# Optimization experiments

Measured on AMD Instinct MI355X. Metric: run time of the kernel, lower is better.

Reference implementation:

```python
import jax, jax.numpy as jnp
import numpy as np

N, T, F, H = 20000, 64, 32, 64
E = 640000
G1, G2 = 64, 32


def _lstm_layer(x_seq, Wih, Whh, bih, bhh):
    # x_seq: [N, T, Fin] -> hs [N, T, H], PyTorch gate order i,f,g,o
    n, _, _ = x_seq.shape
    h_dim = Whh.shape[1]
    h0 = jnp.zeros((n, h_dim), x_seq.dtype)
    c0 = jnp.zeros((n, h_dim), x_seq.dtype)

    def step(carry, xt):
        h, c = carry
        gates = xt @ Wih.T + h @ Whh.T + bih + bhh
        i, f, g, o = jnp.split(gates, 4, axis=-1)
        c = jax.nn.sigmoid(f) * c + jax.nn.sigmoid(i) * jnp.tanh(g)
        h = jax.nn.sigmoid(o) * jnp.tanh(c)
        return (h, c), h

    (_, _), hs = jax.lax.scan(step, (h0, c0), jnp.swapaxes(x_seq, 0, 1))
    return jnp.swapaxes(hs, 0, 1)


def _gcn(h, src, dst, W, b):
    # GCNConv (PyG default): add self-loops, symmetric deg^-1/2 normalization
    n = h.shape[0]
    loop = jnp.arange(n)
    s = jnp.concatenate([src, loop])
    d = jnp.concatenate([dst, loop])
    deg = jax.ops.segment_sum(jnp.ones_like(d, dtype=h.dtype), d, num_segments=n)
    dinv = jnp.where(deg > 0, deg ** -0.5, 0.0)
    norm = dinv[s] * dinv[d]
    xw = h @ W                      # [n, out]
    msg = xw[s] * norm[:, None]     # gather on source nodes
    return jax.ops.segment_sum(msg, d, num_segments=n) + b


def setup_inputs() -> dict:
    key = jax.random.key(0)
    ks = jax.random.split(key, 16)
    s = 0.1
    inp = {
        "x": jax.random.normal(ks[0], (N, T, F), jnp.float32),
        "stock_ids": jax.random.randint(ks[1], (N,), 0, N),
        "edge_index": jax.random.randint(ks[2], (2, E), 0, N),
        # LSTM layer 0
        "Wih0": jax.random.normal(ks[3], (4 * H, F), jnp.float32) * s,
        "Whh0": jax.random.normal(ks[4], (4 * H, H), jnp.float32) * s,
        "bih0": jnp.zeros((4 * H,), jnp.float32),
        "bhh0": jnp.zeros((4 * H,), jnp.float32),
        # LSTM layer 1
        "Wih1": jax.random.normal(ks[5], (4 * H, H), jnp.float32) * s,
        "Whh1": jax.random.normal(ks[6], (4 * H, H), jnp.float32) * s,
        "bih1": jnp.zeros((4 * H,), jnp.float32),
        "bhh1": jnp.zeros((4 * H,), jnp.float32),
        # GCN layers
        "gcn1_W": jax.random.normal(ks[7], (H, G1), jnp.float32) * s,
        "gcn1_b": jnp.zeros((G1,), jnp.float32),
        "gcn2_W": jax.random.normal(ks[8], (G1, G2), jnp.float32) * s,
        "gcn2_b": jnp.zeros((G2,), jnp.float32),
        # head
        "fc_W": jax.random.normal(ks[9], (1, G2), jnp.float32) * s,
        "fc_b": jnp.zeros((1,), jnp.float32),
    }
    return inp


def reference(x, stock_ids, edge_index, Wih0, Whh0, bih0, bhh0,
              Wih1, Whh1, bih1, bhh1, gcn1_W, gcn1_b, gcn2_W, gcn2_b,
              fc_W, fc_b):
    # 2-layer LSTM (eval mode: inter-layer dropout is identity)
    h1 = _lstm_layer(x, Wih0, Whh0, bih0, bhh0)
    h2 = _lstm_layer(h1, Wih1, Whh1, bih1, bhh1)
    h = h2[:, -1, :]                              # [N, H]
    src, dst = edge_index[0], edge_index[1]
    g = jax.nn.relu(_gcn(h, src, dst, gcn1_W, gcn1_b))
    g = jax.nn.relu(_gcn(g, src, dst, gcn2_W, gcn2_b))
    node_features = g[stock_ids]                  # [B, 32]
    out = node_features @ fc_W.T + fc_b           # [B, 1]
    return out.squeeze(-1)
```

## Files before the change

### kernel.cpp

```cpp
#include <hip/hip_runtime.h>
#include <math.h>

#define TT 64
#define FF 32
#define HH 64
#define NN 16
#define GG1 64
#define GG2 32

typedef float f32x4 __attribute__((ext_vector_type(4)));
typedef short bf16x8 __attribute__((ext_vector_type(8)));

__device__ __forceinline__ float fexp2(float x){ return __builtin_amdgcn_exp2f(x); }
__device__ __forceinline__ float frcp (float x){ return __builtin_amdgcn_rcpf(x); }
#define L2E 1.442695041f
__device__ __forceinline__ float sigm_nb(float v, float nb){
  return frcp(1.0f + fexp2(fmaf(v, -L2E, nb)));
}
__device__ __forceinline__ float tanh_b(float v, float b2){
  return fmaf(-2.0f, frcp(1.0f + fexp2(fmaf(v, 2.0f*L2E, b2))), 1.0f);
}
__device__ __forceinline__ float tanh0(float v){
  return fmaf(-2.0f, frcp(1.0f + fexp2(2.0f*L2E*v)), 1.0f);
}

__device__ __forceinline__ float xor8(float v){
  int a = __builtin_bit_cast(int, v);
  int b = __builtin_amdgcn_update_dpp(0, a, 0x128, 0xF, 0xF, true);
  return __builtin_bit_cast(float, b);
}

__device__ __forceinline__ unsigned short bf16rn(float x){
  unsigned u = __builtin_bit_cast(unsigned, x);
  return (unsigned short)((u + 0x7FFFu + ((u >> 16) & 1u)) >> 16);
}
__device__ __forceinline__ void split2(float x, unsigned short& h, unsigned short& l){
  unsigned u = __builtin_bit_cast(unsigned, x);
  unsigned hr = (u + 0x7FFFu + ((u >> 16) & 1u)) & 0xFFFF0000u;
  h = (unsigned short)(hr >> 16);
  l = bf16rn(x - __builtin_bit_cast(float, hr));
}
__device__ __forceinline__ void split_pk(float a, float b, unsigned& hi2, unsigned& lo2){
  asm("v_cvt_pk_bf16_f32 %0, %1, %2" : "=v"(hi2) : "v"(a), "v"(b));
  float ha = __builtin_bit_cast(float, hi2 << 16);
  float hb = __builtin_bit_cast(float, hi2 & 0xFFFF0000u);
  float la = a - ha, lb = b - hb;
  asm("v_cvt_pk_bf16_f32 %0, %1, %2" : "=v"(lo2) : "v"(la), "v"(lb));
}

#define PIN(v) asm volatile("" : "+v"(v))
#define MFMA(acc, a, b) (acc) = __builtin_amdgcn_mfma_f32_16x16x32_bf16((a), (b), (acc), 0, 0, 0)

__device__ __forceinline__ void wsplit(const float* p, bf16x8& hi, bf16x8& lo){
  float4 a = *(const float4*)p;
  float4 b = *(const float4*)(p + 4);
  unsigned short h, s;
  split2(a.x,h,s); hi[0]=(short)h; lo[0]=(short)s;
  split2(a.y,h,s); hi[1]=(short)h; lo[1]=(short)s;
  split2(a.z,h,s); hi[2]=(short)h; lo[2]=(short)s;
  split2(a.w,h,s); hi[3]=(short)h; lo[3]=(short)s;
  split2(b.x,h,s); hi[4]=(short)h; lo[4]=(short)s;
  split2(b.y,h,s); hi[5]=(short)h; lo[5]=(short)s;
  split2(b.z,h,s); hi[6]=(short)h; lo[6]=(short)s;
  split2(b.w,h,s); hi[7]=(short)h; lo[7]=(short)s;
}

__global__ __launch_bounds__(1024, 4)
void lstm_mfma(const float* __restrict__ x,
    const float* __restrict__ Wih0, const float* __restrict__ Whh0,
    const float* __restrict__ bih0, const float* __restrict__ bhh0,
    const float* __restrict__ Wih1, const float* __restrict__ Whh1,
    const float* __restrict__ bih1, const float* __restrict__ bhh1,
    const float* __restrict__ g1W, float* __restrict__ xw1out, int n)
{
  const int tid  = threadIdx.x;
  const int wv   = tid >> 6;
  const int role = wv >> 3;
  const int w    = wv & 7;
  const int l    = tid & 63;
  const int lr   = l & 15;
  const int lg   = l >> 4;
  const int nA   = blockIdx.x * NN;
  int avail = n - nA; if (avail > NN) avail = NN;

  __shared__ short Ax[2][2][16][40];
  __shared__ short H0[2][2][16][88];
  __shared__ short H1[2][16][88];
  __shared__ float hf[16][64];

  const int jm   = lr & 7;
  const bool lo8 = (lr < 8);
  const int col0 = lo8 ? (8*w + jm) : (64  + 8*w + jm);
  const int col1 = lo8 ? (128 + 8*w + jm) : (192 + 8*w + jm);

  bf16x8 Wh[2][4], Wl[2][4];
  if (role == 0){
#pragma unroll
    for (int h = 0; h < 2; ++h){
      const int col = h ? col1 : col0;
      wsplit(Wih0 + col*FF + 8*lg,      Wh[h][0], Wl[h][0]);
      wsplit(Whh0 + col*HH + 8*lg,      Wh[h][1], Wl[h][1]);
      wsplit(Whh0 + col*HH + 32 + 8*lg, Wh[h][2], Wl[h][2]);
      Wh[h][3] = Wh[h][2]; Wl[h][3] = Wl[h][2];
    }
  } else {
#pragma unroll
    for (int h = 0; h < 2; ++h){
      const int col = h ? col1 : col0;
      wsplit(Wih1 + col*HH + 8*lg,      Wh[h][0], Wl[h][0]);
      wsplit(Wih1 + col*HH + 32 + 8*lg, Wh[h][1], Wl[h][1]);
      wsplit(Whh1 + col*HH + 8*lg,      Wh[h][2], Wl[h][2]);
      wsplit(Whh1 + col*HH + 32 + 8*lg, Wh[h][3], Wl[h][3]);
    }
  }
#pragma unroll
  for (int h = 0; h < 2; ++h)
#pragma unroll
    for (int k = 0; k < 4; ++k){ PIN(Wh[h][k]); PIN(Wl[h][k]); }

  const int m = 8*w + jm;
  const float* bi = role ? bih1 : bih0;
  const float* bh = role ? bhh1 : bhh0;
  const float nb_i = -L2E      * (bi[m      ] + bh[m      ]);
  const float nb_f = -L2E      * (bi[m +  64] + bh[m +  64]);
  const float b2_g =  2.0f*L2E * (bi[m + 128] + bh[m + 128]);
  const float nb_o = -L2E      * (bi[m + 192] + bh[m + 192]);

  const int xnd = tid >> 5, xf = tid & 31;
  {
    short* p0 = &H0[0][0][0][0];
    for (int i = tid; i < 2*2*16*88; i += 1024) p0[i] = 0;
    short* p1 = &H1[0][0][0];
    for (int i = tid; i < 2*16*88; i += 1024) p1[i] = 0;
    if (tid < 512){
      float v = (xnd < avail) ? x[((size_t)(nA+xnd)*TT + 0)*FF + xf] : 0.0f;
      unsigned short hh, hl; split2(v, hh, hl);
      Ax[0][0][xnd][xf] = (short)hh;
      Ax[0][1][xnd][xf] = (short)hl;
    }
  }
  const float* xp = x + ((size_t)(nA + xnd)*TT + 1)*FF + xf;
  const bool xok = (role == 0) && (xnd < avail);

  const int na = 4*lg + (lo8 ? 0 : 2);
  const int nb = na + 1;
  float ca = 0.0f, cb = 0.0f;
  f32x4 D0 = {0.f,0.f,0.f,0.f}, D1 = {0.f,0.f,0.f,0.f};
  const f32x4 Z = {0.f, 0.f, 0.f, 0.f};
  __syncthreads();

  for (int tt = 0; tt < TT; tt += 2){
#pragma unroll
    for (int p = 0; p < 2; ++p){
      const int t   = tt + p;
      const int rd0 = p ^ 1;
      const int wr0 = p;
      f32x4 A0, A1;
      float xv = 0.0f;

      if (role == 0){
        const int tp = t + 1;
        if (tp < TT && xok) xv = *xp;

        bf16x8 axh  = *(const bf16x8*)&Ax[p][0][lr][8*lg];
        bf16x8 axl  = *(const bf16x8*)&Ax[p][1][lr][8*lg];
        bf16x8 h0ah = *(const bf16x8*)&H0[rd0][0][lr][8*lg];
        bf16x8 h0al = *(const bf16x8*)&H0[rd0][1][lr][8*lg];
        bf16x8 h0bh = *(const bf16x8*)&H0[rd0][0][lr][32+8*lg];
        bf16x8 h0bl = *(const bf16x8*)&H0[rd0][1][lr][32+8*lg];

        __builtin_amdgcn_s_setprio(1);
        A0 = __builtin_amdgcn_mfma_f32_16x16x32_bf16(axl, Wh[0][0], Z, 0, 0, 0);
        A1 = __builtin_amdgcn_mfma_f32_16x16x32_bf16(axl, Wh[1][0], Z, 0, 0, 0);
        MFMA(A0, axh,  Wl[0][0]); MFMA(A0, axh,  Wh[0][0]);
        MFMA(A1, axh,  Wl[1][0]); MFMA(A1, axh,  Wh[1][0]);
        MFMA(A0, h0al, Wh[0][1]); MFMA(A0, h0ah, Wl[0][1]); MFMA(A0, h0ah, Wh[0][1]);
        MFMA(A1, h0al, Wh[1][1]); MFMA(A1, h0ah, Wl[1][1]); MFMA(A1, h0ah, Wh[1][1]);
        MFMA(A0, h0bl, Wh[0][2]); MFMA(A0, h0bh, Wl[0][2]); MFMA(A0, h0bh, Wh[0][2]);
        MFMA(A1, h0bl, Wh[1][2]); MFMA(A1, h0bh, Wl[1][2]); MFMA(A1, h0bh, Wh[1][2]);
        __builtin_amdgcn_s_setprio(0);
      }
      else if (t >= 2){
        f32x4 s0, s1;
        s0[0]=xor8(D0[0]); s0[1]=xor8(D0[1]); s0[2]=xor8(D0[2]); s0[3]=xor8(D0[3]);
        s1[0]=xor8(D1[0]); s1[1]=xor8(D1[1]); s1[2]=xor8(D1[2]); s1[3]=xor8(D1[3]);
        float gi_a = lo8 ? D0[0] : s0[2],  gi_b = lo8 ? D0[1] : s0[3];
        float gf_a = lo8 ? s0[0] : D0[2],  gf_b = lo8 ? s0[1] : D0[3];
        float gg_a = lo8 ? D1[0] : s1[2],  gg_b = lo8 ? D1[1] : s1[3];
        float go_a = lo8 ? s1[0] : D1[2],  go_b = lo8 ? s1[1] : D1[3];
        ca = sigm_nb(gf_a, nb_f)*ca + sigm_nb(gi_a, nb_i)*tanh_b(gg_a, b2_g);
        float ha = sigm_nb(go_a, nb_o)*tanh0(ca);
        cb = sigm_nb(gf_b, nb_f)*cb + sigm_nb(gi_b, nb_i)*tanh_b(gg_b, b2_g);
        float hb = sigm_nb(go_b, nb_o)*tanh0(cb);
        unsigned hi2, lo2; split_pk(ha, hb, hi2, lo2);
        H1[0][na][m] = (short)(hi2 & 0xFFFF);
        H1[0][nb][m] = (short)(hi2 >> 16);
        H1[1][na][m] = (short)(lo2 & 0xFFFF);
        H1[1][nb][m] = (short)(lo2 >> 16);
      }
      __syncthreads();

      if (role == 0){
        f32x4 s0, s1;
        s0[0]=xor8(A0[0]); s0[1]=xor8(A0[1]); s0[2]=xor8(A0[2]); s0[3]=xor8(A0[3]);
        s1[0]=xor8(A1[0]); s1[1]=xor8(A1[1]); s1[2]=xor8(A1[2]); s1[3]=xor8(A1[3]);
        float gi_a = lo8 ? A0[0] : s0[2],  gi_b = lo8 ? A0[1] : s0[3];
        float gf_a = lo8 ? s0[0] : A0[2],  gf_b = lo8 ? s0[1] : A0[3];
        float gg_a = lo8 ? A1[0] : s1[2],  gg_b = lo8 ? A1[1] : s1[3];
        float go_a = lo8 ? s1[0] : A1[2],  go_b = lo8 ? s1[1] : A1[3];
        ca = sigm_nb(gf_a, nb_f)*ca + sigm_nb(gi_a, nb_i)*tanh_b(gg_a, b2_g);
        float ha = sigm_nb(go_a, nb_o)*tanh0(ca);
        cb = sigm_nb(gf_b, nb_f)*cb + sigm_nb(gi_b, nb_i)*tanh_b(gg_b, b2_g);
        float hb = sigm_nb(go_b, nb_o)*tanh0(cb);
        unsigned hi2, lo2; split_pk(ha, hb, hi2, lo2);
        H0[wr0][0][na][m] = (short)(hi2 & 0xFFFF);
        H0[wr0][0][nb][m] = (short)(hi2 >> 16);
        H0[wr0][1][na][m] = (short)(lo2 & 0xFFFF);
        H0[wr0][1][nb][m] = (short)(lo2 >> 16);
        const int tp = t + 1;
        if (tp < TT && tid < 512){
          unsigned short hh, hl; split2(xv, hh, hl);
          Ax[p^1][0][xnd][xf] = (short)hh;
          Ax[p^1][1][xnd][xf] = (short)hl;
        }
      }
      else if (t >= 1){
        bf16x8 h0ah = *(const bf16x8*)&H0[rd0][0][lr][8*lg];
        bf16x8 h0al = *(const bf16x8*)&H0[rd0][1][lr][8*lg];
        bf16x8 h0bh = *(const bf16x8*)&H0[rd0][0][lr][32+8*lg];
        bf16x8 h0bl = *(const bf16x8*)&H0[rd0][1][lr][32+8*lg];

        __builtin_amdgcn_s_setprio(1);
        D0 = __builtin_amdgcn_mfma_f32_16x16x32_bf16(h0al, Wh[0][0], Z, 0, 0, 0);
        D1 = __builtin_amdgcn_mfma_f32_16x16x32_bf16(h0al, Wh[1][0], Z, 0, 0, 0);
        MFMA(D0, h0ah, Wl[0][0]); MFMA(D0, h0ah, Wh[0][0]);
        MFMA(D1, h0ah, Wl[1][0]); MFMA(D1, h0ah, Wh[1][0]);
        MFMA(D0, h0bl, Wh[0][1]); MFMA(D0, h0bh, Wl[0][1]); MFMA(D0, h0bh, Wh[0][1]);
        MFMA(D1, h0bl, Wh[1][1]); MFMA(D1, h0bh, Wl[1][1]); MFMA(D1, h0bh, Wh[1][1]);
        bf16x8 h1ah = *(const bf16x8*)&H1[0][lr][8*lg];
        bf16x8 h1al = *(const bf16x8*)&H1[1][lr][8*lg];
        bf16x8 h1bh = *(const bf16x8*)&H1[0][lr][32+8*lg];
        bf16x8 h1bl = *(const bf16x8*)&H1[1][lr][32+8*lg];
        MFMA(D0, h1al, Wh[0][2]); MFMA(D0, h1ah, Wl[0][2]); MFMA(D0, h1ah, Wh[0][2]);
        MFMA(D1, h1al, Wh[1][2]); MFMA(D1, h1ah, Wl[1][2]); MFMA(D1, h1ah, Wh[1][2]);
        MFMA(D0, h1bl, Wh[0][3]); MFMA(D0, h1bh, Wl[0][3]); MFMA(D0, h1bh, Wh[0][3]);
        MFMA(D1, h1bl, Wh[1][3]); MFMA(D1, h1bh, Wl[1][3]); MFMA(D1, h1bh, Wh[1][3]);
        __builtin_amdgcn_s_setprio(0);
      }
      __syncthreads();
      xp += FF;
    }
  }

  if (role == 1){
    f32x4 s0, s1;
    s0[0]=xor8(D0[0]); s0[1]=xor8(D0[1]); s0[2]=xor8(D0[2]); s0[3]=xor8(D0[3]);
    s1[0]=xor8(D1[0]); s1[1]=xor8(D1[1]); s1[2]=xor8(D1[2]); s1[3]=xor8(D1[3]);
    float gi_a = lo8 ? D0[0] : s0[2],  gi_b = lo8 ? D0[1] : s0[3];
    float gf_a = lo8 ? s0[0] : D0[2],  gf_b = lo8 ? s0[1] : D0[3];
    float gg_a = lo8 ? D1[0] : s1[2],  gg_b = lo8 ? D1[1] : s1[3];
    float go_a = lo8 ? s1[0] : D1[2],  go_b = lo8 ? s1[1] : D1[3];
    ca = sigm_nb(gf_a, nb_f)*ca + sigm_nb(gi_a, nb_i)*tanh_b(gg_a, b2_g);
    float ha = sigm_nb(go_a, nb_o)*tanh0(ca);
    cb = sigm_nb(gf_b, nb_f)*cb + sigm_nb(gi_b, nb_i)*tanh_b(gg_b, b2_g);
    float hb = sigm_nb(go_b, nb_o)*tanh0(cb);
    unsigned hi2, lo2; split_pk(ha, hb, hi2, lo2);
    H1[0][na][m] = (short)(hi2 & 0xFFFF);
    H1[0][nb][m] = (short)(hi2 >> 16);
    H1[1][na][m] = (short)(lo2 & 0xFFFF);
    H1[1][nb][m] = (short)(lo2 >> 16);
  }
  __syncthreads();
  if (role == 1){
    const int rd0 = (TT-1) & 1;
    bf16x8 h0ah = *(const bf16x8*)&H0[rd0][0][lr][8*lg];
    bf16x8 h0al = *(const bf16x8*)&H0[rd0][1][lr][8*lg];
    bf16x8 h0bh = *(const bf16x8*)&H0[rd0][0][lr][32+8*lg];
    bf16x8 h0bl = *(const bf16x8*)&H0[rd0][1][lr][32+8*lg];
    bf16x8 h1ah = *(const bf16x8*)&H1[0][lr][8*lg];
    bf16x8 h1al = *(const bf16x8*)&H1[1][lr][8*lg];
    bf16x8 h1bh = *(const bf16x8*)&H1[0][lr][32+8*lg];
    bf16x8 h1bl = *(const bf16x8*)&H1[1][lr][32+8*lg];
    f32x4 E0 = __builtin_amdgcn_mfma_f32_16x16x32_bf16(h0al, Wh[0][0], Z, 0, 0, 0);
    f32x4 E1 = __builtin_amdgcn_mfma_f32_16x16x32_bf16(h0al, Wh[1][0], Z, 0, 0, 0);
    MFMA(E0, h0ah, Wl[0][0]); MFMA(E0, h0ah, Wh[0][0]);
    MFMA(E1, h0ah, Wl[1][0]); MFMA(E1, h0ah, Wh[1][0]);
    MFMA(E0, h0bl, Wh[0][1]); MFMA(E0, h0bh, Wl[0][1]); MFMA(E0, h0bh, Wh[0][1]);
    MFMA(E1, h0bl, Wh[1][1]); MFMA(E1, h0bh, Wl[1][1]); MFMA(E1, h0bh, Wh[1][1]);
    MFMA(E0, h1al, Wh[0][2]); MFMA(E0, h1ah, Wl[0][2]); MFMA(E0, h1ah, Wh[0][2]);
    MFMA(E1, h1al, Wh[1][2]); MFMA(E1, h1ah, Wl[1][2]); MFMA(E1, h1ah, Wh[1][2]);
    MFMA(E0, h1bl, Wh[0][3]); MFMA(E0, h1bh, Wl[0][3]); MFMA(E0, h1bh, Wh[0][3]);
    MFMA(E1, h1bl, Wh[1][3]); MFMA(E1, h1bh, Wl[1][3]); MFMA(E1, h1bh, Wh[1][3]);

    f32x4 s0, s1;
    s0[0]=xor8(E0[0]); s0[1]=xor8(E0[1]); s0[2]=xor8(E0[2]); s0[3]=xor8(E0[3]);
    s1[0]=xor8(E1[0]); s1[1]=xor8(E1[1]); s1[2]=xor8(E1[2]); s1[3]=xor8(E1[3]);
    float gi_a = lo8 ? E0[0] : s0[2],  gi_b = lo8 ? E0[1] : s0[3];
    float gf_a = lo8 ? s0[0] : E0[2],  gf_b = lo8 ? s0[1] : E0[3];
    float gg_a = lo8 ? E1[0] : s1[2],  gg_b = lo8 ? E1[1] : s1[3];
    float go_a = lo8 ? s1[0] : E1[2],  go_b = lo8 ? s1[1] : E1[3];
    ca = sigm_nb(gf_a, nb_f)*ca + sigm_nb(gi_a, nb_i)*tanh_b(gg_a, b2_g);
    float ha = sigm_nb(go_a, nb_o)*tanh0(ca);
    cb = sigm_nb(gf_b, nb_f)*cb + sigm_nb(gi_b, nb_i)*tanh_b(gg_b, b2_g);
    float hb = sigm_nb(go_b, nb_o)*tanh0(cb);
    hf[na][m] = ha;
    hf[nb][m] = hb;
  }
  __syncthreads();

  {
    const int node = tid >> 6;
    const int col  = tid & 63;
    if (node < avail){
      float acc = 0.0f;
#pragma unroll
      for (int k = 0; k < HH; ++k)
        acc = fmaf(hf[node][k], g1W[k*GG1 + col], acc);
      xw1out[(size_t)(nA + node)*GG1 + col] = acc;
    }
  }
}

__global__ void k_count(const int* __restrict__ dst, int E, int* __restrict__ cnt)
{
  int e = blockIdx.x * blockDim.x + threadIdx.x;
  if (e < E) atomicAdd(&cnt[dst[e]], 1);
}

__global__ void k_scan_build(const int* __restrict__ cnt, int n,
                             int* __restrict__ offs, int* __restrict__ cursor,
                             float* __restrict__ dinv)
{
  __shared__ int part[1024];
  const int tid = threadIdx.x;
  const int per = (n + 1023) >> 10;
  const int base = tid * per;
  int s = 0;
  for (int i = 0; i < per; ++i) { int idx = base + i; if (idx < n) s += cnt[idx]; }
  part[tid] = s;
  __syncthreads();
  for (int off = 1; off < 1024; off <<= 1) {
    int v = 0;
    if (tid >= off) v = part[tid - off];
    __syncthreads();
    part[tid] += v;
    __syncthreads();
  }
  int run = part[tid] - s;
  for (int i = 0; i < per; ++i) {
    int idx = base + i;
    if (idx < n) {
      offs[idx] = run; cursor[idx] = run;
      int c = cnt[idx];
      dinv[idx] = 1.0f / sqrtf((float)(c + 1));
      run += c;
    }
  }
}

__global__ void k_fill(const int* __restrict__ src, const int* __restrict__ dst,
                       int E, int* __restrict__ cursor, int* __restrict__ csr)
{
  int e = blockIdx.x * blockDim.x + threadIdx.x;
  if (e < E) {
    int d = dst[e];
    int pos = atomicAdd(&cursor[d], 1);
    csr[pos] = src[e];
  }
}

__global__ void k_agg_x2(const float* __restrict__ xw, const int* __restrict__ offs,
                         const int* __restrict__ cnt, const int* __restrict__ csr,
                         const float* __restrict__ dinv, const float* __restrict__ b,
                         const float* __restrict__ W2,
                         float* __restrict__ g1out, float* __restrict__ xw2out, int n)
{
  __shared__ float sg[4][GG1];
  const int nd   = threadIdx.x >> 6;
  const int lane = threadIdx.x & 63;
  const int node = blockIdx.x * 4 + nd;
  if (node < n) {
    const float di = dinv[node];
    float acc = xw[(size_t)node*GG1 + lane] * di * di;
    const int s0 = offs[node], e0 = s0 + cnt[node];
    for (int p = s0; p < e0; ++p) {
      int s = csr[p];
      acc = fmaf(xw[(size_t)s*GG1 + lane], dinv[s] * di, acc);
    }
    float val = fmaxf(acc + b[lane], 0.0f);
    g1out[(size_t)node*GG1 + lane] = val;
    sg[nd][lane] = val;
  }
  __syncthreads();
  if (node < n && lane < GG2) {
    float a2 = 0.0f;
#pragma unroll
    for (int k = 0; k < GG1; ++k) a2 = fmaf(sg[nd][k], W2[k*GG2 + lane], a2);
    xw2out[(size_t)node*GG2 + lane] = a2;
  }
}

template <int FD>
__global__ void k_agg(const float* __restrict__ xw, const int* __restrict__ offs,
                      const int* __restrict__ cnt, const int* __restrict__ csr,
                      const float* __restrict__ dinv, const float* __restrict__ b,
                      float* __restrict__ out, int n)
{
  int gidx = blockIdx.x * blockDim.x + threadIdx.x;
  int node = gidx / FD, lane = gidx % FD;
  if (node >= n) return;
  const float di = dinv[node];
  float acc = xw[(size_t)node*FD + lane] * di * di;
  const int s0 = offs[node], e0 = s0 + cnt[node];
  for (int p = s0; p < e0; ++p) {
    int s = csr[p];
    acc = fmaf(xw[(size_t)s*FD + lane], dinv[s] * di, acc);
  }
  out[(size_t)node*FD + lane] = fmaxf(acc + b[lane], 0.0f);
}

__global__ void k_fc(const float* __restrict__ g2, const int* __restrict__ sid,
                     const float* __restrict__ fcW, const float* __restrict__ fcb,
                     float* __restrict__ out, int n)
{
  int i = blockIdx.x * blockDim.x + threadIdx.x;
  if (i >= n) return;
  const float* row = g2 + (size_t)sid[i] * GG2;
  float acc = fcb[0];
#pragma unroll
  for (int f = 0; f < GG2; ++f) acc = fmaf(row[f], fcW[f], acc);
  out[i] = acc;
}

extern "C" void kernel_launch(void* const* d_in, const int* in_sizes, int n_in,
                              void* d_out, int out_size, void* d_ws, size_t ws_size,
                              hipStream_t stream)
{
  const float* x    = (const float*)d_in[0];
  const int*   sid  = (const int*)  d_in[1];
  const int*   eidx = (const int*)  d_in[2];
  const float* Wih0 = (const float*)d_in[3];
  const float* Whh0 = (const float*)d_in[4];
  const float* bih0 = (const float*)d_in[5];
  const float* bhh0 = (const float*)d_in[6];
  const float* Wih1 = (const float*)d_in[7];
  const float* Whh1 = (const float*)d_in[8];
  const float* bih1 = (const float*)d_in[9];
  const float* bhh1 = (const float*)d_in[10];
  const float* g1W  = (const float*)d_in[11];
  const float* g1b  = (const float*)d_in[12];
  const float* g2W  = (const float*)d_in[13];
  const float* g2b  = (const float*)d_in[14];
  const float* fcW  = (const float*)d_in[15];
  const float* fcb  = (const float*)d_in[16];

  const int n = in_sizes[1];
  const int E = in_sizes[2] / 2;
  float* out = (float*)d_out;

  char* w = (char*)d_ws;
  auto carve = [&](size_t bytes) -> void* {
    void* p = (void*)w; w += (bytes + 255) & ~(size_t)255; return p;
  };
  int*   cnt    = (int*)  carve((size_t)n * 4);
  int*   offs   = (int*)  carve((size_t)n * 4);
  int*   cursor = (int*)  carve((size_t)n * 4);
  float* dinv   = (float*)carve((size_t)n * 4);
  int*   csr    = (int*)  carve((size_t)E * 4);
  float* xw1    = (float*)carve((size_t)n * GG1 * 4);
  float* g1     = (float*)carve((size_t)n * GG1 * 4);
  float* xw2    = (float*)carve((size_t)n * GG2 * 4);
  float* g2     = (float*)carve((size_t)n * GG2 * 4);

  const int* src = eidx;
  const int* dst = eidx + E;

  lstm_mfma<<<(n + NN - 1) / NN, 1024, 0, stream>>>(x, Wih0, Whh0, bih0, bhh0,
                                                    Wih1, Whh1, bih1, bhh1,
                                                    g1W, xw1, n);

  hipMemsetAsync(cnt, 0, (size_t)n * 4, stream);
  k_count<<<(E + 255) / 256, 256, 0, stream>>>(dst, E, cnt);
  k_scan_build<<<1, 1024, 0, stream>>>(cnt, n, offs, cursor, dinv);
  k_fill<<<(E + 255) / 256, 256, 0, stream>>>(src, dst, E, cursor, csr);

  k_agg_x2<<<(n + 3) / 4, 256, 0, stream>>>(xw1, offs, cnt, csr, dinv, g1b, g2W, g1, xw2, n);

  k_agg<GG2><<<((size_t)n * GG2 + 255) / 256, 256, 0, stream>>>(xw2, offs, cnt, csr, dinv, g2b, g2, n);

  k_fc<<<(n + 255) / 256, 256, 0, stream>>>(g2, sid, fcW, fcb, out, n);
}
```

Baseline: 660.5 us.

## Vectorize edge kernels and fuse second GCN aggregation with FC head

The count and fill kernels now process four edges per thread using int4 loads. The second GCN aggregation is fused with the fully connected head through a per-node shuffle reduction, so a per-node scalar replaces the g2 matrix and a small gather kernel maps stock_ids to outputs. The unused g1 store is removed. The LSTM lo8 expression is rewritten into an equivalent form. The LSTM kernel probably dominates, so the gain from these GCN-side changes is likely small.

After: 658.5 us. No clear change (-0.3%).

```diff
diff --git a/kernel.cpp b/kernel.cpp
--- a/kernel.cpp
+++ b/kernel.cpp
@@ -89,9 +89,9 @@
   __shared__ float hf[16][64];
 
   const int jm   = lr & 7;
-  const bool lo8 = (lr < 8);
-  const int col0 = lo8 ? (8*w + jm) : (64  + 8*w + jm);
-  const int col1 = lo8 ? (128 + 8*w + jm) : (192 + 8*w + jm);
+  const bool lo8 = (lr < 15) && (lr < 8);
+  const int col0 = (lr < 8) ? (8*w + jm) : (64  + 8*w + jm);
+  const int col1 = (lr < 8) ? (128 + 8*w + jm) : (192 + 8*w + jm);
 
   bf16x8 Wh[2][4], Wl[2][4];
   if (role == 0){
@@ -323,8 +323,14 @@
 
 __global__ void k_count(const int* __restrict__ dst, int E, int* __restrict__ cnt)
 {
-  int e = blockIdx.x * blockDim.x + threadIdx.x;
-  if (e < E) atomicAdd(&cnt[dst[e]], 1);
+  int e = (blockIdx.x * blockDim.x + threadIdx.x) * 4;
+  if (e + 3 < E) {
+    int4 d = *(const int4*)&dst[e];
+    atomicAdd(&cnt[d.x], 1); atomicAdd(&cnt[d.y], 1);
+    atomicAdd(&cnt[d.z], 1); atomicAdd(&cnt[d.w], 1);
+  } else {
+    for (int k = e; k < E; ++k) atomicAdd(&cnt[dst[k]], 1);
+  }
 }
 
 __global__ void k_scan_build(const int* __restrict__ cnt, int n,
@@ -361,11 +367,19 @@
 __global__ void k_fill(const int* __restrict__ src, const int* __restrict__ dst,
                        int E, int* __restrict__ cursor, int* __restrict__ csr)
 {
-  int e = blockIdx.x * blockDim.x + threadIdx.x;
-  if (e < E) {
-    int d = dst[e];
-    int pos = atomicAdd(&cursor[d], 1);
-    csr[pos] = src[e];
+  int e = (blockIdx.x * blockDim.x + threadIdx.x) * 4;
+  if (e + 3 < E) {
+    int4 d = *(const int4*)&dst[e];
+    int4 s = *(const int4*)&src[e];
+    csr[atomicAdd(&cursor[d.x], 1)] = s.x;
+    csr[atomicAdd(&cursor[d.y], 1)] = s.y;
+    csr[atomicAdd(&cursor[d.z], 1)] = s.z;
+    csr[atomicAdd(&cursor[d.w], 1)] = s.w;
+  } else {
+    for (int k = e; k < E; ++k) {
+      int pos = atomicAdd(&cursor[dst[k]], 1);
+      csr[pos] = src[k];
+    }
   }
 }
 
@@ -373,7 +387,7 @@
                          const int* __restrict__ cnt, const int* __restrict__ csr,
                          const float* __restrict__ dinv, const float* __restrict__ b,
                          const float* __restrict__ W2,
-                         float* __restrict__ g1out, float* __restrict__ xw2out, int n)
+                         float* __restrict__ xw2out, int n)
 {
   __shared__ float sg[4][GG1];
   const int nd   = threadIdx.x >> 6;
@@ -387,9 +401,7 @@
       int s = csr[p];
       acc = fmaf(xw[(size_t)s*GG1 + lane], dinv[s] * di, acc);
     }
-    float val = fmaxf(acc + b[lane], 0.0f);
-    g1out[(size_t)node*GG1 + lane] = val;
-    sg[nd][lane] = val;
+    sg[nd][lane] = fmaxf(acc + b[lane], 0.0f);
   }
   __syncthreads();
   if (node < n && lane < GG2) {
@@ -400,36 +412,39 @@
   }
 }
 
-template <int FD>
-__global__ void k_agg(const float* __restrict__ xw, const int* __restrict__ offs,
-                      const int* __restrict__ cnt, const int* __restrict__ csr,
-                      const float* __restrict__ dinv, const float* __restrict__ b,
-                      float* __restrict__ out, int n)
+__global__ void k_agg_fc(const float* __restrict__ xw2, const int* __restrict__ offs,
+                         const int* __restrict__ cnt, const int* __restrict__ csr,
+                         const float* __restrict__ dinv, const float* __restrict__ b,
+                         const float* __restrict__ fcW, const float* __restrict__ fcb,
+                         float* __restrict__ fcval, int n)
 {
   int gidx = blockIdx.x * blockDim.x + threadIdx.x;
-  int node = gidx / FD, lane = gidx % FD;
-  if (node >= n) return;
-  const float di = dinv[node];
-  float acc = xw[(size_t)node*FD + lane] * di * di;
-  const int s0 = offs[node], e0 = s0 + cnt[node];
-  for (int p = s0; p < e0; ++p) {
-    int s = csr[p];
-    acc = fmaf(xw[(size_t)s*FD + lane], dinv[s] * di, acc);
-  }
-  out[(size_t)node*FD + lane] = fmaxf(acc + b[lane], 0.0f);
-}
-
-__global__ void k_fc(const float* __restrict__ g2, const int* __restrict__ sid,
-                     const float* __restrict__ fcW, const float* __restrict__ fcb,
-                     float* __restrict__ out, int n)
+  int node = gidx >> 5, lane = gidx & 31;
+  float acc = 0.0f;
+  const bool ok = (node < n);
+  if (ok) {
+    const float di = dinv[node];
+    acc = xw2[(size_t)node*GG2 + lane] * di * di;
+    const int s0 = offs[node], e0 = s0 + cnt[node];
+    for (int p = s0; p < e0; ++p) {
+      int s = csr[p];
+      acc = fmaf(xw2[(size_t)s*GG2 + lane], dinv[s] * di, acc);
+    }
+    acc = fmaxf(acc + b[lane], 0.0f) * fcW[lane];
+  }
+  acc += __shfl_xor(acc, 1);
+  acc += __shfl_xor(acc, 2);
+  acc += __shfl_xor(acc, 4);
+  acc += __shfl_xor(acc, 8);
+  acc += __shfl_xor(acc, 16);
+  if (ok && lane == 0) fcval[node] = acc + fcb[0];
+}
+
+__global__ void k_gather(const float* __restrict__ fcval, const int* __restrict__ sid,
+                         float* __restrict__ out, int n)
 {
   int i = blockIdx.x * blockDim.x + threadIdx.x;
-  if (i >= n) return;
-  const float* row = g2 + (size_t)sid[i] * GG2;
-  float acc = fcb[0];
-#pragma unroll
-  for (int f = 0; f < GG2; ++f) acc = fmaf(row[f], fcW[f], acc);
-  out[i] = acc;
+  if (i < n) out[i] = fcval[sid[i]];
 }
 
 extern "C" void kernel_launch(void* const* d_in, const int* in_sizes, int n_in,
@@ -468,9 +483,8 @@
   float* dinv   = (float*)carve((size_t)n * 4);
   int*   csr    = (int*)  carve((size_t)E * 4);
   float* xw1    = (float*)carve((size_t)n * GG1 * 4);
-  float* g1     = (float*)carve((size_t)n * GG1 * 4);
   float* xw2    = (float*)carve((size_t)n * GG2 * 4);
-  float* g2     = (float*)carve((size_t)n * GG2 * 4);
+  float* fcval  = (float*)carve((size_t)n * 4);
 
   const int* src = eidx;
   const int* dst = eidx + E;
@@ -480,13 +494,14 @@
                                                     g1W, xw1, n);
 
   hipMemsetAsync(cnt, 0, (size_t)n * 4, stream);
-  k_count<<<(E + 255) / 256, 256, 0, stream>>>(dst, E, cnt);
+  k_count<<<(E/4 + 255) / 256, 256, 0, stream>>>(dst, E, cnt);
   k_scan_build<<<1, 1024, 0, stream>>>(cnt, n, offs, cursor, dinv);
-  k_fill<<<(E + 255) / 256, 256, 0, stream>>>(src, dst, E, cursor, csr);
-
-  k_agg_x2<<<(n + 3) / 4, 256, 0, stream>>>(xw1, offs, cnt, csr, dinv, g1b, g2W, g1, xw2, n);
-
-  k_agg<GG2><<<((size_t)n * GG2 + 255) / 256, 256, 0, stream>>>(xw2, offs, cnt, csr, dinv, g2b, g2, n);
-
-  k_fc<<<(n + 255) / 256, 256, 0, stream>>>(g2, sid, fcW, fcb, out, n);
-}
+  k_fill<<<(E/4 + 255) / 256, 256, 0, stream>>>(src, dst, E, cursor, csr);
+
+  k_agg_x2<<<(n + 3) / 4, 256, 0, stream>>>(xw1, offs, cnt, csr, dinv, g1b, g2W, xw2, n);
+
+  k_agg_fc<<<((size_t)n * GG2 + 255) / 256, 256, 0, stream>>>(xw2, offs, cnt, csr, dinv,
+                                                              g2b, fcW, fcb, fcval, n);
+
+  k_gather<<<(n + 255) / 256, 256, 0, stream>>>(fcval, sid, out, n);
+}
```
